# Kernel optimization log

Hardware: AMD Instinct MI355X
Metric: run time of the kernel (lower is better)

Reference implementation:

```python
import jax, jax.numpy as jnp
import numpy as np

NEG = -10000000.0

def setup_inputs() -> dict:
    key0 = jax.random.key(0)
    ks = jax.random.split(key0, 5)
    B, XL, KL, D = 16, 1024, 512, 1024  # D = 2*rnn_dim
    return {
        "x": jax.random.normal(ks[0], (B, XL, D), dtype=jnp.float32),
        "x_mask": jnp.ones((B, XL), dtype=jnp.float32),
        "key": jax.random.normal(ks[1], (B, KL, D), dtype=jnp.float32),
        "key_mask": jnp.ones((B, KL), dtype=jnp.float32),
        "w_input": jax.random.normal(ks[2], (D,), dtype=jnp.float32) / np.sqrt(D),
        "w_key": jax.random.normal(ks[3], (D,), dtype=jnp.float32) / np.sqrt(D),
        "dot_w": jax.random.normal(ks[4], (D,), dtype=jnp.float32) / np.sqrt(D),
    }

def reference(x, x_mask, key, key_mask, w_input, w_key, dot_w):
    # Trilinear attention score S[b,i,j] = w_in.x_i + w_key.k_j + (x_i*dot_w).k_j
    x_logits = jnp.einsum('bxd,d->bx', x, w_input)      # [B, XL]
    key_logits = jnp.einsum('bkd,d->bk', key, w_key)    # [B, KL]
    S = (x_logits[:, :, None] + key_logits[:, None, :]
         + jnp.einsum('bxd,bkd->bxk', x * dot_w, key))  # [B, XL, KL]

    # x -> key attention with joint mask
    joint_mask = 1.0 - x_mask[:, :, None] * key_mask[:, None, :]
    masked_S = S + joint_mask * NEG
    attn = jax.nn.softmax(masked_S, axis=-1)
    x2key = jnp.einsum('bxk,bkd->bxd', attn, key)       # [B, XL, D]

    # key -> x attention: mask over key dim, max-reduce, masked softmax over x
    km = key_mask[:, None, :]
    S2 = S * km + (1.0 - km) * NEG                      # add_masked_value
    max_s = jnp.max(S2, axis=-1)                        # [B, XL]
    p = jax.nn.softmax(max_s * x_mask, axis=-1) * x_mask  # claf masked_softmax
    p = p / (jnp.sum(p, axis=-1, keepdims=True) + 1e-13)
    key2x = jnp.einsum('bx,bxd->bd', p, x)[:, None, :]  # [B, 1, D], broadcasts

    key2x_full = jnp.broadcast_to(key2x, x.shape)
    return jnp.concatenate([x, x2key, x * x2key, x * key2x_full], axis=-1)
```

## Files before the change

### kernel.cpp

```cpp
#include <hip/hip_runtime.h>
#include <hip/hip_fp16.h>

#define B_ 16
#define XL_ 1024
#define KL_ 512
#define D_ 1024
#define NEGC (-10000000.0f)

typedef _Float16 f16x8 __attribute__((ext_vector_type(8)));
typedef float f32x4 __attribute__((ext_vector_type(4)));
typedef unsigned short u16x8 __attribute__((ext_vector_type(8)));
typedef unsigned short u16x4 __attribute__((ext_vector_type(4)));

__device__ __forceinline__ unsigned short f2h(float f) {
  __half h = __float2half(f);
  return __half_as_ushort(h);
}

__global__ __launch_bounds__(256) void k_prep_x(const float* __restrict__ x,
    const float* __restrict__ w_input, float* __restrict__ xlog) {
  int wv = threadIdx.x >> 6, lane = threadIdx.x & 63;
  int row = blockIdx.x * 4 + wv;
  const float* src = x + (size_t)row * D_;
  float acc = 0.f;
#pragma unroll
  for (int j = 0; j < 4; ++j) {
    int d = j * 256 + lane * 4;
    float4 v = *(const float4*)(src + d);
    float4 w = *(const float4*)(w_input + d);
    acc += v.x * w.x + v.y * w.y + v.z * w.z + v.w * w.w;
  }
#pragma unroll
  for (int sh = 32; sh >= 1; sh >>= 1) acc += __shfl_xor(acc, sh);
  if (lane == 0) xlog[row] = acc;
}

__global__ __launch_bounds__(256) void k_build(const float* __restrict__ key,
    const float* __restrict__ w_key, unsigned short* __restrict__ KQ2,
    unsigned short* __restrict__ KV2, float* __restrict__ klog) {
  __shared__ unsigned short tile[64][72];
  int b = blockIdx.x >> 3, ks = blockIdx.x & 7;
  int tid = threadIdx.x;
  int kr = tid >> 2;
  int cq = tid & 3;
  const float* krow = key + ((size_t)(b * KL_ + ks * 64 + kr)) * D_;
  float klacc = 0.f;
  int dl = tid & 63, g = tid >> 6;

  for (int dt = 0; dt < 16; ++dt) {
#pragma unroll
    for (int j = 0; j < 4; ++j) {
      int c = dt * 64 + cq * 16 + j * 4;
      float4 v = *(const float4*)(krow + c);
      float4 w = *(const float4*)(w_key + c);
      klacc += v.x * w.x + v.y * w.y + v.z * w.z + v.w * w.w;
      u16x4 hv;
      hv[0] = f2h(v.x); hv[1] = f2h(v.y); hv[2] = f2h(v.z); hv[3] = f2h(v.w);
      *(u16x4*)(&tile[kr][cq * 16 + j * 4]) = hv;
    }
    __syncthreads();
#pragma unroll
    for (int dkc_l = 0; dkc_l < 2; ++dkc_l) {
      u16x8 hv = *(const u16x8*)(&tile[kr][dkc_l * 32 + cq * 8]);
      size_t dst = (((size_t)(b * 8 + ks) * 32 + (dt * 2 + dkc_l)) << 11)
                   + (size_t)(((kr >> 4) & 3) * 512 + (cq * 16 + (kr & 15)) * 8);
      *(u16x8*)(KQ2 + dst) = hv;
    }
    {
      int dglob = dt * 64 + dl;
      int wv_ = dglob >> 7, np = (dglob >> 4) & 7, l15v = dglob & 15;
#pragma unroll
      for (int kkc_l = 0; kkc_l < 2; ++kkc_l) {
        u16x8 hv;
#pragma unroll
        for (int h = 0; h < 8; ++h) hv[h] = tile[kkc_l * 32 + g * 8 + h][dl];
        size_t dst = (((size_t)(b * 8 + wv_) * 16 + (ks * 2 + kkc_l)) << 12)
                     + (size_t)(np * 512 + (g * 16 + l15v) * 8);
        *(u16x8*)(KV2 + dst) = hv;
      }
    }
    __syncthreads();
  }
  klacc += __shfl_xor(klacc, 1);
  klacc += __shfl_xor(klacc, 2);
  if (cq == 0) klog[b * KL_ + ks * 64 + kr] = klacc;
}

__global__ __launch_bounds__(512, 4) void k_attn(
    const float* __restrict__ x, const float* __restrict__ x_mask,
    const float* __restrict__ key_mask, const float* __restrict__ dot_w,
    const unsigned short* __restrict__ KQ2, const unsigned short* __restrict__ KV2,
    const float* __restrict__ xlog, const float* __restrict__ klog,
    float* __restrict__ maxs, float* __restrict__ out) {
  __shared__ unsigned short Qall[32 * 1024];
  unsigned short* Pt = Qall;
  float* redA = (float*)(Qall + 16384);
  float* redB = redA + 256;
  float* redC = redB + 256;

  const int tid = threadIdx.x;
  const int wv = tid >> 6;
  const int lane = tid & 63;
  const int l15 = lane & 15, l4 = lane >> 4;
  const int r7 = l15 & 7;

  int bid = blockIdx.x;
  int b = (bid & 7) * 2 + (bid >> 8);
  int x0 = ((bid >> 3) & 31) * 32;

  const float* xB = x + ((size_t)b * XL_ + x0) * D_;

  {
    int row = tid >> 4;
    int cg = tid & 15;
    const float* sp = xB + (size_t)row * D_;
    char* qrow = (char*)Qall + row * 2048;
    int rsw = row & 7;
#pragma unroll
    for (int j = 0; j < 16; ++j) {
      int c4 = cg + j * 16;
      float4 v = *(const float4*)(sp + c4 * 4);
      float4 w = *(const float4*)(dot_w + c4 * 4);
      u16x4 hv;
      hv[0] = f2h(v.x * w.x); hv[1] = f2h(v.y * w.y);
      hv[2] = f2h(v.z * w.z); hv[3] = f2h(v.w * w.w);
      *(u16x4*)(qrow + (((c4 >> 1) ^ rsw) << 4) + ((c4 & 1) << 3)) = hv;
    }
  }
  __syncthreads();

  f32x4 acc[2][4];
#pragma unroll
  for (int m = 0; m < 2; ++m)
#pragma unroll
    for (int n = 0; n < 4; ++n) { f32x4 z = {0.f, 0.f, 0.f, 0.f}; acc[m][n] = z; }

  const unsigned short* KQ2w = KQ2 + (((size_t)(b * 8 + wv) * 32) << 11) + lane * 8;
  const char* qa0 = (char*)Qall + l15 * 2048;
  const char* qa1 = (char*)Qall + (16 + l15) * 2048;

#pragma unroll 2
  for (int dk = 0; dk < D_; dk += 32) {
    const unsigned short* cp = KQ2w + ((dk >> 5) << 11);
    f16x8 b0 = *(const f16x8*)(cp);
    f16x8 b1 = *(const f16x8*)(cp + 512);
    f16x8 b2 = *(const f16x8*)(cp + 1024);
    f16x8 b3 = *(const f16x8*)(cp + 1536);
    int c = (((dk >> 3) + l4) ^ r7) << 4;
    f16x8 a0 = *(const f16x8*)(qa0 + c);
    f16x8 a1 = *(const f16x8*)(qa1 + c);
    __builtin_amdgcn_s_setprio(1);
    acc[0][0] = __builtin_amdgcn_mfma_f32_16x16x32_f16(b0, a0, acc[0][0], 0, 0, 0);
    acc[1][0] = __builtin_amdgcn_mfma_f32_16x16x32_f16(b0, a1, acc[1][0], 0, 0, 0);
    acc[0][1] = __builtin_amdgcn_mfma_f32_16x16x32_f16(b1, a0, acc[0][1], 0, 0, 0);
    acc[1][1] = __builtin_amdgcn_mfma_f32_16x16x32_f16(b1, a1, acc[1][1], 0, 0, 0);
    acc[0][2] = __builtin_amdgcn_mfma_f32_16x16x32_f16(b2, a0, acc[0][2], 0, 0, 0);
    acc[1][2] = __builtin_amdgcn_mfma_f32_16x16x32_f16(b2, a1, acc[1][2], 0, 0, 0);
    acc[0][3] = __builtin_amdgcn_mfma_f32_16x16x32_f16(b3, a0, acc[0][3], 0, 0, 0);
    acc[1][3] = __builtin_amdgcn_mfma_f32_16x16x32_f16(b3, a1, acc[1][3], 0, 0, 0);
    __builtin_amdgcn_s_setprio(0);
  }
  __syncthreads();

  float xlv[2], xmv[2];
#pragma unroll
  for (int m = 0; m < 2; ++m) {
    int row = m * 16 + l15;
    xlv[m] = xlog[(size_t)b * XL_ + x0 + row];
    xmv[m] = x_mask[(size_t)b * XL_ + x0 + row];
  }
  f32x4 klv[4], kmv[4];
#pragma unroll
  for (int n = 0; n < 4; ++n) {
    int kb = wv * 64 + n * 16 + l4 * 4;
    klv[n] = *(const f32x4*)(klog + (size_t)b * KL_ + kb);
    kmv[n] = *(const f32x4*)(key_mask + (size_t)b * KL_ + kb);
  }
  float mxsm[2] = {-3.0e38f, -3.0e38f}, mxs2[2] = {-3.0e38f, -3.0e38f};
#pragma unroll
  for (int m = 0; m < 2; ++m)
#pragma unroll
    for (int n = 0; n < 4; ++n)
#pragma unroll
      for (int q = 0; q < 4; ++q) {
        float s = acc[m][n][q] + xlv[m] + klv[n][q];
        float sm = s + (1.f - xmv[m] * kmv[n][q]) * NEGC;
        float s2 = s * kmv[n][q] + (1.f - kmv[n][q]) * NEGC;
        mxsm[m] = fmaxf(mxsm[m], sm);
        mxs2[m] = fmaxf(mxs2[m], s2);
      }
#pragma unroll
  for (int m = 0; m < 2; ++m) {
    mxsm[m] = fmaxf(mxsm[m], __shfl_xor(mxsm[m], 16));
    mxsm[m] = fmaxf(mxsm[m], __shfl_xor(mxsm[m], 32));
    mxs2[m] = fmaxf(mxs2[m], __shfl_xor(mxs2[m], 16));
    mxs2[m] = fmaxf(mxs2[m], __shfl_xor(mxs2[m], 32));
  }
  if (l4 == 0) {
#pragma unroll
    for (int m = 0; m < 2; ++m) {
      redA[wv * 32 + m * 16 + l15] = mxsm[m];
      redB[wv * 32 + m * 16 + l15] = mxs2[m];
    }
  }
  __syncthreads();
  float gmx[2];
#pragma unroll
  for (int m = 0; m < 2; ++m) {
    int row = m * 16 + l15;
    float v = redA[row];
#pragma unroll
    for (int w = 1; w < 8; ++w) v = fmaxf(v, redA[w * 32 + row]);
    gmx[m] = v;
  }
  if (tid < 32) {
    float v = redB[tid];
#pragma unroll
    for (int w = 1; w < 8; ++w) v = fmaxf(v, redB[w * 32 + tid]);
    maxs[(size_t)b * XL_ + x0 + tid] = v;
  }
  float rs[2] = {0.f, 0.f};
#pragma unroll
  for (int m = 0; m < 2; ++m) {
    int row = m * 16 + l15;
    char* prow = (char*)Pt + row * 1024;
    int rsw = row & 7;
#pragma unroll
    for (int n = 0; n < 4; ++n) {
      int k = wv * 64 + n * 16 + l4 * 4;
      u16x4 pk;
#pragma unroll
      for (int q = 0; q < 4; ++q) {
        float s = acc[m][n][q] + xlv[m] + klv[n][q];
        float sm = s + (1.f - xmv[m] * kmv[n][q]) * NEGC;
        float e = __expf(sm - gmx[m]);
        rs[m] += e;
        pk[q] = f2h(e);
      }
      *(u16x4*)(prow + ((((k >> 3) ^ rsw) << 4) + ((k & 4) << 1))) = pk;
    }
  }
#pragma unroll
  for (int m = 0; m < 2; ++m) {
    rs[m] += __shfl_xor(rs[m], 16);
    rs[m] += __shfl_xor(rs[m], 32);
  }
  if (l4 == 0) {
#pragma unroll
    for (int m = 0; m < 2; ++m) redC[wv * 32 + m * 16 + l15] = rs[m];
  }
  __syncthreads();

  float dn[2];
#pragma unroll
  for (int m = 0; m < 2; ++m) {
    int row = m * 16 + l15;
    float sum = redC[row];
#pragma unroll
    for (int w = 1; w < 8; ++w) sum += redC[w * 32 + row];
    dn[m] = 1.f / sum;
  }
  size_t obase0 = ((size_t)b * XL_ + x0) * (size_t)(4 * D_);
  const char* pa0 = (char*)Pt + l15 * 1024;
  const char* pa1 = (char*)Pt + (16 + l15) * 1024;
  const unsigned short* KV2w = KV2 + (((size_t)(b * 8 + wv) * 16) << 12) + lane * 8;
#pragma unroll
  for (int sc = 0; sc < 2; ++sc) {
    int c0 = wv * 128 + sc * 64;
    f32x4 acc2[2][4];
#pragma unroll
    for (int m = 0; m < 2; ++m)
#pragma unroll
      for (int n = 0; n < 4; ++n) { f32x4 z = {0.f, 0.f, 0.f, 0.f}; acc2[m][n] = z; }
    const unsigned short* KV2s = KV2w + sc * 4 * 512;
#pragma unroll 2
    for (int kk = 0; kk < KL_; kk += 32) {
      const unsigned short* cp = KV2s + ((kk >> 5) << 12);
      f16x8 b0 = *(const f16x8*)(cp);
      f16x8 b1 = *(const f16x8*)(cp + 512);
      f16x8 b2 = *(const f16x8*)(cp + 1024);
      f16x8 b3 = *(const f16x8*)(cp + 1536);
      int c = ((((kk >> 3) + l4) ^ r7) << 4);
      f16x8 a0 = *(const f16x8*)(pa0 + c);
      f16x8 a1 = *(const f16x8*)(pa1 + c);
      __builtin_amdgcn_s_setprio(1);
      acc2[0][0] = __builtin_amdgcn_mfma_f32_16x16x32_f16(b0, a0, acc2[0][0], 0, 0, 0);
      acc2[1][0] = __builtin_amdgcn_mfma_f32_16x16x32_f16(b0, a1, acc2[1][0], 0, 0, 0);
      acc2[0][1] = __builtin_amdgcn_mfma_f32_16x16x32_f16(b1, a0, acc2[0][1], 0, 0, 0);
      acc2[1][1] = __builtin_amdgcn_mfma_f32_16x16x32_f16(b1, a1, acc2[1][1], 0, 0, 0);
      acc2[0][2] = __builtin_amdgcn_mfma_f32_16x16x32_f16(b2, a0, acc2[0][2], 0, 0, 0);
      acc2[1][2] = __builtin_amdgcn_mfma_f32_16x16x32_f16(b2, a1, acc2[1][2], 0, 0, 0);
      acc2[0][3] = __builtin_amdgcn_mfma_f32_16x16x32_f16(b3, a0, acc2[0][3], 0, 0, 0);
      acc2[1][3] = __builtin_amdgcn_mfma_f32_16x16x32_f16(b3, a1, acc2[1][3], 0, 0, 0);
      __builtin_amdgcn_s_setprio(0);
    }
#pragma unroll
    for (int m = 0; m < 2; ++m) {
      int row = m * 16 + l15;
      size_t ob = obase0 + (size_t)row * (4 * D_);
      const float* xr = xB + (size_t)row * D_;
#pragma unroll
      for (int n = 0; n < 4; ++n) {
        int col = c0 + n * 16 + l4 * 4;
        f32x4 v = acc2[m][n];
        v[0] *= dn[m]; v[1] *= dn[m]; v[2] *= dn[m]; v[3] *= dn[m];
        f32x4 xv = *(const f32x4*)(xr + col);
        *(f32x4*)(out + ob + col) = xv;
        *(f32x4*)(out + ob + D_ + col) = v;
        f32x4 pv;
        pv[0] = v[0] * xv[0]; pv[1] = v[1] * xv[1];
        pv[2] = v[2] * xv[2]; pv[3] = v[3] * xv[3];
        *(f32x4*)(out + ob + 2 * D_ + col) = pv;
      }
    }
  }
}

__global__ __launch_bounds__(256) void k_p(const float* __restrict__ maxs,
    const float* __restrict__ x_mask, float* __restrict__ pbuf) {
  int b = blockIdx.x, tid = threadIdx.x;
  int wv = tid >> 6, lane = tid & 63;
  __shared__ float r1[4], r2[4], r3[4];
  const float* ms = maxs + (size_t)b * XL_;
  const float* xm = x_mask + (size_t)b * XL_;
  float tv[4], xmv[4];
  float vmax = -3.0e38f;
#pragma unroll
  for (int i = 0; i < 4; ++i) {
    int xi = i * 256 + tid;
    xmv[i] = xm[xi];
    tv[i] = ms[xi] * xmv[i];
    vmax = fmaxf(vmax, tv[i]);
  }
#pragma unroll
  for (int sh = 32; sh >= 1; sh >>= 1) vmax = fmaxf(vmax, __shfl_xor(vmax, sh));
  if (lane == 0) r1[wv] = vmax;
  __syncthreads();
  float gmax = fmaxf(fmaxf(r1[0], r1[1]), fmaxf(r1[2], r1[3]));
  float e[4]; float es = 0.f;
#pragma unroll
  for (int i = 0; i < 4; ++i) { e[i] = __expf(tv[i] - gmax); es += e[i]; }
#pragma unroll
  for (int sh = 32; sh >= 1; sh >>= 1) es += __shfl_xor(es, sh);
  if (lane == 0) r2[wv] = es;
  __syncthreads();
  float gsum = r2[0] + r2[1] + r2[2] + r2[3];
  float pv[4]; float ps = 0.f;
#pragma unroll
  for (int i = 0; i < 4; ++i) { pv[i] = e[i] / gsum * xmv[i]; ps += pv[i]; }
#pragma unroll
  for (int sh = 32; sh >= 1; sh >>= 1) ps += __shfl_xor(ps, sh);
  if (lane == 0) r3[wv] = ps;
  __syncthreads();
  float gps = r3[0] + r3[1] + r3[2] + r3[3];
  float inv = 1.f / (gps + 1e-13f);
#pragma unroll
  for (int i = 0; i < 4; ++i) pbuf[(size_t)b * XL_ + i * 256 + tid] = pv[i] * inv;
}

__global__ __launch_bounds__(256) void k_key2x_part(const float* __restrict__ x,
    const float* __restrict__ pbuf, float* __restrict__ partial) {
  int b = blockIdx.x >> 4;
  int xc = blockIdx.x & 15;
  __shared__ float ps[64];
  if (threadIdx.x < 64) ps[threadIdx.x] = pbuf[(size_t)b * XL_ + xc * 64 + threadIdx.x];
  __syncthreads();
  const float* xb = x + ((size_t)b * XL_ + xc * 64) * D_;
  float acc0 = 0.f, acc1 = 0.f, acc2 = 0.f, acc3 = 0.f;
  int d = threadIdx.x;
  for (int xi = 0; xi < 64; ++xi) {
    float pv = ps[xi];
    const float* rp = xb + (size_t)xi * D_;
    acc0 += pv * rp[d];
    acc1 += pv * rp[d + 256];
    acc2 += pv * rp[d + 512];
    acc3 += pv * rp[d + 768];
  }
  float* pp = partial + (size_t)blockIdx.x * D_;
  pp[d] = acc0; pp[d + 256] = acc1; pp[d + 512] = acc2; pp[d + 768] = acc3;
}

__global__ __launch_bounds__(256) void k_key2x_red(const float* __restrict__ partial,
    float* __restrict__ k2x) {
  int idx = blockIdx.x * 256 + threadIdx.x;
  int b = idx >> 10;
  float s = 0.f;
#pragma unroll
  for (int xc = 0; xc < 16; ++xc)
    s += partial[((size_t)b * 16 + xc) * D_ + (idx & 1023)];
  k2x[idx] = s;
}

__global__ __launch_bounds__(256) void k_outfinal(const float* __restrict__ x,
    const float* __restrict__ k2x, float* __restrict__ out) {
  size_t t = (size_t)blockIdx.x * 256 + threadIdx.x;
  size_t base = t * 4;
  int b = (int)(base >> 20);
  int rem = (int)(base & ((1u << 20) - 1));
  int xr = rem >> 10;
  int d = rem & 1023;
  float4 xv = *(const float4*)(x + base);
  float4 kv = *(const float4*)(k2x + (size_t)b * D_ + d);
  float* orow = out + ((size_t)b * XL_ + xr) * (size_t)(4 * D_);
  float4 pr;
  pr.x = xv.x * kv.x; pr.y = xv.y * kv.y; pr.z = xv.z * kv.z; pr.w = xv.w * kv.w;
  *(float4*)(orow + 3 * D_ + d) = pr;
}

extern "C" void kernel_launch(void* const* d_in, const int* in_sizes, int n_in,
                              void* d_out, int out_size, void* d_ws, size_t ws_size,
                              hipStream_t stream) {
  (void)in_sizes; (void)n_in; (void)out_size; (void)ws_size;
  const float* x        = (const float*)d_in[0];
  const float* x_mask   = (const float*)d_in[1];
  const float* key      = (const float*)d_in[2];
  const float* key_mask = (const float*)d_in[3];
  const float* w_input  = (const float*)d_in[4];
  const float* w_key    = (const float*)d_in[5];
  const float* dot_w    = (const float*)d_in[6];
  float* out = (float*)d_out;
  char* ws = (char*)d_ws;

  unsigned short* KQ2 = (unsigned short*)ws;
  unsigned short* KV2 = (unsigned short*)(ws + (16u << 20));
  float* xlog = (float*)(ws + (32u << 20));
  float* klog = xlog + B_ * XL_;
  float* maxs = klog + B_ * KL_;
  float* pbuf = maxs + B_ * XL_;
  float* k2x  = pbuf + B_ * XL_;
  float* partial = (float*)ws;

  k_build<<<dim3(B_ * 8), dim3(256), 0, stream>>>(key, w_key, KQ2, KV2, klog);
  k_prep_x<<<dim3(B_ * XL_ / 4), dim3(256), 0, stream>>>(x, w_input, xlog);
  k_attn<<<dim3(512), dim3(512), 0, stream>>>(x, x_mask, key_mask, dot_w,
                                              KQ2, KV2, xlog, klog, maxs, out);
  k_p<<<dim3(B_), dim3(256), 0, stream>>>(maxs, x_mask, pbuf);
  k_key2x_part<<<dim3(B_ * 16), dim3(256), 0, stream>>>(x, pbuf, partial);
  k_key2x_red<<<dim3(B_ * D_ / 256), dim3(256), 0, stream>>>(partial, k2x);
  k_outfinal<<<dim3(B_ * XL_ * D_ / 1024), dim3(256), 0, stream>>>(x, k2x, out);
}
```

Baseline: 181.3 us.

## Fuse x-logit dot product into attention kernel and split key build over D halves

Removes the separate k_prep_x pass by computing w_input·x inside k_attn while x is already being loaded to build the fp16 query tile, and keeps the row logits in shared memory. Splits k_build across two D halves to double its grid (128 to 256 blocks), accumulating key logits with atomicAdd after a memset of klog. Also raises the unroll factor of both MFMA loops from 2 to 4. This saves one full read of x and one launch, at the cost of an extra memset, atomics, and possibly more register pressure in k_attn.

```diff
diff --git a/kernel.cpp b/kernel.cpp
--- a/kernel.cpp
+++ b/kernel.cpp
@@ -17,29 +17,14 @@
   return __half_as_ushort(h);
 }
 
-__global__ __launch_bounds__(256) void k_prep_x(const float* __restrict__ x,
-    const float* __restrict__ w_input, float* __restrict__ xlog) {
-  int wv = threadIdx.x >> 6, lane = threadIdx.x & 63;
-  int row = blockIdx.x * 4 + wv;
-  const float* src = x + (size_t)row * D_;
-  float acc = 0.f;
-#pragma unroll
-  for (int j = 0; j < 4; ++j) {
-    int d = j * 256 + lane * 4;
-    float4 v = *(const float4*)(src + d);
-    float4 w = *(const float4*)(w_input + d);
-    acc += v.x * w.x + v.y * w.y + v.z * w.z + v.w * w.w;
-  }
-#pragma unroll
-  for (int sh = 32; sh >= 1; sh >>= 1) acc += __shfl_xor(acc, sh);
-  if (lane == 0) xlog[row] = acc;
-}
-
 __global__ __launch_bounds__(256) void k_build(const float* __restrict__ key,
     const float* __restrict__ w_key, unsigned short* __restrict__ KQ2,
     unsigned short* __restrict__ KV2, float* __restrict__ klog) {
   __shared__ unsigned short tile[64][72];
-  int b = blockIdx.x >> 3, ks = blockIdx.x & 7;
+  int bid = blockIdx.x;
+  int b = bid >> 4;
+  int ks = (bid >> 1) & 7;
+  int dh = bid & 1;
   int tid = threadIdx.x;
   int kr = tid >> 2;
   int cq = tid & 3;
@@ -47,7 +32,7 @@
   float klacc = 0.f;
   int dl = tid & 63, g = tid >> 6;
 
-  for (int dt = 0; dt < 16; ++dt) {
+  for (int dt = dh * 8; dt < dh * 8 + 8; ++dt) {
 #pragma unroll
     for (int j = 0; j < 4; ++j) {
       int c = dt * 64 + cq * 16 + j * 4;
@@ -83,16 +68,18 @@
   }
   klacc += __shfl_xor(klacc, 1);
   klacc += __shfl_xor(klacc, 2);
-  if (cq == 0) klog[b * KL_ + ks * 64 + kr] = klacc;
+  if (cq == 0) atomicAdd(&klog[b * KL_ + ks * 64 + kr], klacc);
 }
 
 __global__ __launch_bounds__(512, 4) void k_attn(
     const float* __restrict__ x, const float* __restrict__ x_mask,
     const float* __restrict__ key_mask, const float* __restrict__ dot_w,
+    const float* __restrict__ w_input,
     const unsigned short* __restrict__ KQ2, const unsigned short* __restrict__ KV2,
-    const float* __restrict__ xlog, const float* __restrict__ klog,
+    const float* __restrict__ klog,
     float* __restrict__ maxs, float* __restrict__ out) {
   __shared__ unsigned short Qall[32 * 1024];
+  __shared__ float xlg[32];
   unsigned short* Pt = Qall;
   float* redA = (float*)(Qall + 16384);
   float* redB = redA + 256;
@@ -116,16 +103,24 @@
     const float* sp = xB + (size_t)row * D_;
     char* qrow = (char*)Qall + row * 2048;
     int rsw = row & 7;
+    float xl = 0.f;
 #pragma unroll
     for (int j = 0; j < 16; ++j) {
       int c4 = cg + j * 16;
       float4 v = *(const float4*)(sp + c4 * 4);
       float4 w = *(const float4*)(dot_w + c4 * 4);
+      float4 wi = *(const float4*)(w_input + c4 * 4);
+      xl += v.x * wi.x + v.y * wi.y + v.z * wi.z + v.w * wi.w;
       u16x4 hv;
       hv[0] = f2h(v.x * w.x); hv[1] = f2h(v.y * w.y);
       hv[2] = f2h(v.z * w.z); hv[3] = f2h(v.w * w.w);
       *(u16x4*)(qrow + (((c4 >> 1) ^ rsw) << 4) + ((c4 & 1) << 3)) = hv;
     }
+    xl += __shfl_xor(xl, 1);
+    xl += __shfl_xor(xl, 2);
+    xl += __shfl_xor(xl, 4);
+    xl += __shfl_xor(xl, 8);
+    if (cg == 0) xlg[row] = xl;
   }
   __syncthreads();
 
@@ -139,7 +134,7 @@
   const char* qa0 = (char*)Qall + l15 * 2048;
   const char* qa1 = (char*)Qall + (16 + l15) * 2048;
 
-#pragma unroll 2
+#pragma unroll 4
   for (int dk = 0; dk < D_; dk += 32) {
     const unsigned short* cp = KQ2w + ((dk >> 5) << 11);
     f16x8 b0 = *(const f16x8*)(cp);
@@ -166,7 +161,7 @@
 #pragma unroll
   for (int m = 0; m < 2; ++m) {
     int row = m * 16 + l15;
-    xlv[m] = xlog[(size_t)b * XL_ + x0 + row];
+    xlv[m] = xlg[row];
     xmv[m] = x_mask[(size_t)b * XL_ + x0 + row];
   }
   f32x4 klv[4], kmv[4];
@@ -273,7 +268,7 @@
 #pragma unroll
       for (int n = 0; n < 4; ++n) { f32x4 z = {0.f, 0.f, 0.f, 0.f}; acc2[m][n] = z; }
     const unsigned short* KV2s = KV2w + sc * 4 * 512;
-#pragma unroll 2
+#pragma unroll 4
     for (int kk = 0; kk < KL_; kk += 32) {
       const unsigned short* cp = KV2s + ((kk >> 5) << 12);
       f16x8 b0 = *(const f16x8*)(cp);
@@ -430,10 +425,10 @@
   float* k2x  = pbuf + B_ * XL_;
   float* partial = (float*)ws;
 
-  k_build<<<dim3(B_ * 8), dim3(256), 0, stream>>>(key, w_key, KQ2, KV2, klog);
-  k_prep_x<<<dim3(B_ * XL_ / 4), dim3(256), 0, stream>>>(x, w_input, xlog);
-  k_attn<<<dim3(512), dim3(512), 0, stream>>>(x, x_mask, key_mask, dot_w,
-                                              KQ2, KV2, xlog, klog, maxs, out);
+  hipMemsetAsync(klog, 0, B_ * KL_ * sizeof(float), stream);
+  k_build<<<dim3(B_ * 16), dim3(256), 0, stream>>>(key, w_key, KQ2, KV2, klog);
+  k_attn<<<dim3(512), dim3(512), 0, stream>>>(x, x_mask, key_mask, dot_w, w_input,
+                                              KQ2, KV2, klog, maxs, out);
   k_p<<<dim3(B_), dim3(256), 0, stream>>>(maxs, x_mask, pbuf);
   k_key2x_part<<<dim3(B_ * 16), dim3(256), 0, stream>>>(x, pbuf, partial);
   k_key2x_red<<<dim3(B_ * D_ / 256), dim3(256), 0, stream>>>(partial, k2x);
```

New measurement: 165.9 us. 1.09x faster.
